# Performance work log

Measured on AMD Instinct MI355X. Metric: run time of the kernel, lower is better.

Reference implementation:

```python
import jax, jax.numpy as jnp
import numpy as np

HIDDEN_DIM = 256
N = 8192


def setup_inputs() -> dict:
    key = jax.random.key(0)
    k1, k2, k3, k4 = jax.random.split(key, 4)
    img = jax.random.normal(k1, (N, HIDDEN_DIM), dtype=jnp.float32)
    text = jax.random.normal(k2, (N, HIDDEN_DIM), dtype=jnp.float32)
    # nn.Linear(hidden_dim, hidden_dim, bias=False) weights, shape [out, in]
    scale = 1.0 / np.sqrt(HIDDEN_DIM)
    Wq = jax.random.uniform(k3, (HIDDEN_DIM, HIDDEN_DIM), dtype=jnp.float32, minval=-scale, maxval=scale)
    Wk = jax.random.uniform(k4, (HIDDEN_DIM, HIDDEN_DIM), dtype=jnp.float32, minval=-scale, maxval=scale)
    return {"img": img, "text": text, "Wq": Wq, "Wk": Wk}


def reference(img, text, Wq, Wk):
    d = img.shape[-1]
    norm_fact = 1.0 / jnp.sqrt(jnp.asarray(d, dtype=img.dtype))
    Q = img @ Wq.T                       # [N, D]
    K = text @ Wk.T                      # [N, D]
    scores = Q @ K.T                     # [N, N]
    # softmax over dim=1 (keys), then scaled by 1/sqrt(D)
    attn = jax.nn.softmax(scores, axis=1) * norm_fact
    out_img = attn @ img                 # [N, D]
    out_text = attn @ text               # [N, D]
    return (out_img, out_text)
```

## Files before the change

### kernel.cpp

```cpp
#include <hip/hip_runtime.h>

typedef unsigned short ushort_t;
typedef unsigned int uint_t;
typedef __attribute__((ext_vector_type(8))) short short8;
typedef __attribute__((ext_vector_type(8))) _Float16 half8;
typedef __attribute__((ext_vector_type(4))) _Float16 half4;
typedef __attribute__((ext_vector_type(4))) float float4v;

#define MFMA_BF16(a, b, c) __builtin_amdgcn_mfma_f32_16x16x32_bf16((a), (b), (c), 0, 0, 0)
#define MFMA_F16(a, b, c) __builtin_amdgcn_mfma_f32_16x16x32_f16((a), (b), (c), 0, 0, 0)

#define NQ 8192
#define DIM 256
#define DV 512

__device__ __forceinline__ ushort_t f2bf(float x) {
  union { float f; uint_t u; } v; v.f = x;
  return (ushort_t)((v.u + 0x7fffu + ((v.u >> 16) & 1u)) >> 16);
}
__device__ __forceinline__ float bf2f(ushort_t b) {
  union { uint_t u; float f; } v; v.u = ((uint_t)b) << 16;
  return v.f;
}

__device__ __forceinline__ half8 cvt8h(const float* p) {
  float4v a = *(const float4v*)p;
  float4v b = *(const float4v*)(p + 4);
  half8 r;
  r[0] = (_Float16)a[0]; r[1] = (_Float16)a[1];
  r[2] = (_Float16)a[2]; r[3] = (_Float16)a[3];
  r[4] = (_Float16)b[0]; r[5] = (_Float16)b[1];
  r[6] = (_Float16)b[2]; r[7] = (_Float16)b[3];
  return r;
}

__device__ __forceinline__ half8 as_h8(short8 s) {
  union { short8 s; half8 h; } u; u.s = s; return u.h;
}

__device__ __forceinline__ void load_lds_16(const void* g, void* l) {
  __builtin_amdgcn_global_load_lds(
      (const __attribute__((address_space(1))) uint_t*)g,
      (__attribute__((address_space(3))) uint_t*)l, 16, 0, 0);
}

__device__ __forceinline__ void barrier_vm0_lgkm0() {
  asm volatile("s_waitcnt vmcnt(0) lgkmcnt(0)\ns_barrier" ::: "memory");
}
__device__ __forceinline__ void barrier_lgkm0() {
  asm volatile("s_waitcnt lgkmcnt(0)\ns_barrier" ::: "memory");
}

__global__ __launch_bounds__(256) void wconv_kernel(
    const float* __restrict__ Wq, const float* __restrict__ Wk,
    _Float16* __restrict__ Whq, _Float16* __restrict__ Whk) {
  const int i = (blockIdx.x * 256 + threadIdx.x) * 8;
  half8 q = cvt8h(Wq + i);
  half8 k = cvt8h(Wk + i);
  *(half8*)(Whq + i) = q;
  *(half8*)(Whk + i) = k;
}

__global__ __launch_bounds__(256, 2) void pre_kernel(
    const float* __restrict__ img, const float* __restrict__ text,
    const _Float16* __restrict__ Whq, const _Float16* __restrict__ Whk,
    _Float16* __restrict__ Qh, _Float16* __restrict__ Kh,
    ushort_t* __restrict__ Vt) {
  __shared__ float tile[64][65];
  const int bid = blockIdx.x;
  const int tid = threadIdx.x;
  if (bid < 1024) {
    const int bx = bid & 127;
    const int by = (bid >> 7) & 3;
    const int bz = bid >> 9;
    const int lane = tid & 63;
    const int wv = tid >> 6;
    const int l16 = lane & 15;
    const int quad = lane >> 4;
    const float* A = bz ? text : img;
    const _Float16* W = bz ? Whk : Whq;
    _Float16* C = bz ? Kh : Qh;
    const int row = bx * 64 + wv * 16 + l16;
    const int colbase = by * 64;

    float4v acc[4];
#pragma unroll
    for (int c = 0; c < 4; ++c) acc[c] = (float4v){0.f, 0.f, 0.f, 0.f};
#pragma unroll
    for (int f = 0; f < 8; ++f) {
      const int k0 = f * 32 + quad * 8;
      half8 af = cvt8h(A + (size_t)row * DIM + k0);
#pragma unroll
      for (int c = 0; c < 4; ++c) {
        half8 bfr = *(const half8*)(W + (size_t)(colbase + c * 16 + l16) * DIM + k0);
        acc[c] = MFMA_F16(af, bfr, acc[c]);
      }
    }
    const int rbase = bx * 64 + wv * 16 + quad * 4;
#pragma unroll
    for (int c = 0; c < 4; ++c)
#pragma unroll
      for (int r = 0; r < 4; ++r)
        C[(size_t)(rbase + r) * DIM + colbase + c * 16 + l16] = (_Float16)acc[c][r];
  } else {
    const int vb = bid - 1024;
    const int n0 = (vb & 127) * 64;
    const int c0 = (vb >> 7) * 64;
    const float* src = (c0 < 256) ? img : text;
    const int cc0 = (c0 < 256) ? c0 : (c0 - 256);
#pragma unroll
    for (int i = 0; i < 4; ++i) {
      const int r = i * 16 + (tid >> 4);
      const int c = (tid & 15) * 4;
      *(float4v*)&tile[r][c] = *(const float4v*)(src + (size_t)(n0 + r) * DIM + cc0 + c);
    }
    __syncthreads();
    const int c = tid >> 2;
    const int seg = tid & 3;
    ushort_t tmp[16];
#pragma unroll
    for (int t = 0; t < 16; ++t) tmp[t] = f2bf(tile[seg * 16 + t][c]);
    ushort_t* dst = Vt + (size_t)(c0 + c) * NQ + n0 + seg * 16;
    *(short8*)dst = *(short8*)&tmp[0];
    *(short8*)(dst + 8) = *(short8*)&tmp[8];
  }
}

__device__ __forceinline__ void stage_K(const _Float16* __restrict__ Kh, int k0,
                                        ushort_t* dst, int tid, int wv) {
#pragma unroll
  for (int i = 0; i < 4; ++i) {
    const int chunk = i * 256 + tid;
    const int n = chunk >> 5;
    const int cs = (chunk & 31) ^ (n & 7);
    load_lds_16(Kh + (size_t)(k0 + n) * DIM + cs * 8,
                (char*)dst + (i * 256 + wv * 64) * 16);
  }
}
__device__ __forceinline__ void stage_V(const ushort_t* __restrict__ Vt, int k0,
                                        ushort_t* dst, int tid, int wv) {
#pragma unroll
  for (int i = 0; i < 8; ++i) {
    const int chunk = i * 256 + tid;
    const int vrow = chunk >> 2;
    const int dc = (chunk & 3) ^ ((vrow >> 1) & 3);
    load_lds_16(Vt + (size_t)vrow * NQ + k0 + dc * 8,
                (char*)dst + (i * 256 + wv * 64) * 16);
  }
}

__global__ __launch_bounds__(256, 2) void attn_kernel(
    const _Float16* __restrict__ Qh, const _Float16* __restrict__ Kh,
    const ushort_t* __restrict__ Vt, _Float16* __restrict__ pacc,
    float* __restrict__ pdenom, int kps, int ks) {
  extern __shared__ __align__(16) ushort_t smem[];
  ushort_t* ldsV = smem + 16384;

  const int tid = threadIdx.x;
  const int lane = tid & 63;
  const int wv = tid >> 6;
  const int l16 = lane & 15;
  const int quad = lane >> 4;
  const int id = blockIdx.x;
  const int split = id & (ks - 1);
  const int qtile = id / ks;
  const int kbeg = split * kps;
  const int sw2 = (l16 >> 1) & 3;
  const int swk = l16 & 7;

  short8 qf[8];
  {
    const _Float16* qptr = Qh + (size_t)(qtile * 64 + wv * 16 + l16) * DIM;
#pragma unroll
    for (int f = 0; f < 8; ++f)
      qf[f] = *(const short8*)(qptr + f * 32 + quad * 8);
  }

  float4v acc[4][8];
#pragma unroll
  for (int m = 0; m < 4; ++m)
#pragma unroll
    for (int c = 0; c < 8; ++c) acc[m][c] = (float4v){0.f, 0.f, 0.f, 0.f};
  float dacc[4] = {0.f, 0.f, 0.f, 0.f};

  const int ntiles = kps >> 5;

  stage_K(Kh, kbeg, smem, tid, wv);
  stage_V(Vt, kbeg, ldsV, tid, wv);

  for (int t = 0; t < ntiles; ++t) {
    const ushort_t* Kt = smem + (t & 1) * 8192;
    barrier_vm0_lgkm0();
    if (t + 1 < ntiles)
      stage_K(Kh, kbeg + (t + 1) * 32, smem + ((t + 1) & 1) * 8192, tid, wv);

    if (t > 0) {
      const ushort_t* Pprev = smem + 32768 + ((t - 1) & 1) * 2048;
      short8 pa[4];
#pragma unroll
      for (int m = 0; m < 4; ++m)
        pa[m] = *(const short8*)(Pprev + (m * 16 + l16) * 32 + (quad ^ sw2) * 8);
      __builtin_amdgcn_s_setprio(1);
#pragma unroll
      for (int c = 0; c < 8; ++c) {
        const int vcol = (wv * 8 + c) * 16 + l16;
        short8 vb = *(const short8*)(ldsV + vcol * 32 + (quad ^ sw2) * 8);
#pragma unroll
        for (int m = 0; m < 4; ++m)
          acc[m][c] = MFMA_BF16(pa[m], vb, acc[m][c]);
      }
      __builtin_amdgcn_s_setprio(0);
    }

    float4v s0 = (float4v){0.f, 0.f, 0.f, 0.f};
    float4v s1 = (float4v){0.f, 0.f, 0.f, 0.f};
    __builtin_amdgcn_s_setprio(1);
#pragma unroll
    for (int f = 0; f < 8; ++f) {
      const int cs = ((f * 4 + quad) ^ swk) * 8;
      short8 kb0 = *(const short8*)(Kt + l16 * DIM + cs);
      short8 kb1 = *(const short8*)(Kt + (l16 + 16) * DIM + cs);
      s0 = MFMA_F16(as_h8(qf[f]), as_h8(kb0), s0);
      s1 = MFMA_F16(as_h8(qf[f]), as_h8(kb1), s1);
    }
    __builtin_amdgcn_s_setprio(0);

    barrier_lgkm0();
    if (t >= 1) stage_V(Vt, kbeg + t * 32, ldsV, tid, wv);

    ushort_t* Pcur = smem + 32768 + (t & 1) * 2048;
    ushort_t pb0[4], pb1[4];
#pragma unroll
    for (int r = 0; r < 4; ++r) {
      pb0[r] = f2bf(__expf(s0[r]));
      pb1[r] = f2bf(__expf(s1[r]));
    }
#pragma unroll
    for (int r = 0; r < 4; ++r) {
      const int rb = wv * 16 + quad * 4 + r;
      const int swp = (rb >> 1) & 3;
      Pcur[rb * 32 + ((l16 >> 3) ^ swp) * 8 + (l16 & 7)] = pb0[r];
      Pcur[rb * 32 + ((2 + (l16 >> 3)) ^ swp) * 8 + (l16 & 7)] = pb1[r];
      dacc[r] += bf2f(pb0[r]) + bf2f(pb1[r]);
    }
  }

  barrier_vm0_lgkm0();
  {
    const ushort_t* Pprev = smem + 32768 + ((ntiles - 1) & 1) * 2048;
    short8 pa[4];
#pragma unroll
    for (int m = 0; m < 4; ++m)
      pa[m] = *(const short8*)(Pprev + (m * 16 + l16) * 32 + (quad ^ sw2) * 8);
#pragma unroll
    for (int c = 0; c < 8; ++c) {
      const int vcol = (wv * 8 + c) * 16 + l16;
      short8 vb = *(const short8*)(ldsV + vcol * 32 + (quad ^ sw2) * 8);
#pragma unroll
      for (int m = 0; m < 4; ++m)
        acc[m][c] = MFMA_BF16(pa[m], vb, acc[m][c]);
    }
  }

#pragma unroll
  for (int r = 0; r < 4; ++r) {
    float ts = dacc[r];
    ts += __shfl_xor(ts, 1);
    ts += __shfl_xor(ts, 2);
    ts += __shfl_xor(ts, 4);
    ts += __shfl_xor(ts, 8);
    dacc[r] = ts;
  }

  barrier_lgkm0();
  float* ldsD = (float*)smem;
  if (l16 == 0) {
#pragma unroll
    for (int r = 0; r < 4; ++r)
      ldsD[wv * 16 + quad * 4 + r] = dacc[r];
  }
  barrier_lgkm0();

  _Float16* pout = pacc + (size_t)split * ((size_t)NQ * DV);
#pragma unroll
  for (int m = 0; m < 4; ++m) {
    float invd[4];
#pragma unroll
    for (int r = 0; r < 4; ++r) invd[r] = 1.0f / ldsD[m * 16 + quad * 4 + r];
    const int rowbase = qtile * 64 + m * 16 + quad * 4;
#pragma unroll
    for (int c = 0; c < 8; ++c) {
      const int col = (wv * 8 + c) * 16 + l16;
#pragma unroll
      for (int r = 0; r < 4; ++r)
        pout[(size_t)(rowbase + r) * DV + col] = (_Float16)(acc[m][c][r] * invd[r]);
    }
  }
  if (l16 == 0) {
    const int rowbase = qtile * 64 + wv * 16 + quad * 4;
#pragma unroll
    for (int r = 0; r < 4; ++r)
      pdenom[split * NQ + rowbase + r] = dacc[r];
  }
}

__global__ __launch_bounds__(256) void combine_kernel(
    const _Float16* __restrict__ pacc, const float* __restrict__ pdenom,
    float* __restrict__ out, int ks) {
  const int idx = blockIdx.x * 256 + threadIdx.x;
  const int n = idx >> 6;
  const int c8 = (idx & 63) << 3;
  float s[8] = {0.f, 0.f, 0.f, 0.f, 0.f, 0.f, 0.f, 0.f};
  float dsum = 0.f;
  for (int sp = 0; sp < ks; ++sp) {
    const float d = pdenom[sp * NQ + n];
    half8 x = *(const half8*)(pacc + (size_t)sp * ((size_t)NQ * DV) + (size_t)n * DV + c8);
#pragma unroll
    for (int j = 0; j < 8; ++j) s[j] += d * (float)x[j];
    dsum += d;
  }
  const float scale = 1.0f / (16.0f * dsum);
  float4v lo = (float4v){s[0], s[1], s[2], s[3]} * scale;
  float4v hi = (float4v){s[4], s[5], s[6], s[7]} * scale;
  float* dst = (c8 < 256) ? (out + (size_t)n * DIM + c8)
                          : (out + (size_t)NQ * DIM + (size_t)n * DIM + (c8 - 256));
  *(float4v*)dst = lo;
  *(float4v*)(dst + 4) = hi;
}

extern "C" void kernel_launch(void* const* d_in, const int* in_sizes, int n_in,
                              void* d_out, int out_size, void* d_ws, size_t ws_size,
                              hipStream_t stream) {
  const float* img = (const float*)d_in[0];
  const float* text = (const float*)d_in[1];
  const float* Wq = (const float*)d_in[2];
  const float* Wk = (const float*)d_in[3];
  float* out = (float*)d_out;
  char* ws = (char*)d_ws;

  _Float16* Qh = (_Float16*)ws;
  _Float16* Kh = (_Float16*)(ws + ((size_t)4 << 20));
  ushort_t* Vt = (ushort_t*)(ws + ((size_t)8 << 20));
  const size_t accsz = (size_t)NQ * DV * sizeof(_Float16);
  const size_t base = (size_t)16 << 20;

  int ks = 4;
  if (ws_size < base + 4 * (accsz + NQ * sizeof(float))) ks = 2;
  _Float16* pacc = (_Float16*)(ws + base);
  float* pdenom = (float*)(ws + base + (size_t)ks * accsz);
  _Float16* Whq = (_Float16*)(ws + base);
  _Float16* Whk = Whq + DIM * DIM;

  hipLaunchKernelGGL(wconv_kernel, dim3(32), dim3(256), 0, stream,
                     Wq, Wk, Whq, Whk);
  hipLaunchKernelGGL(pre_kernel, dim3(2048), dim3(256), 0, stream,
                     img, text, Whq, Whk, Qh, Kh, Vt);
  hipLaunchKernelGGL(attn_kernel, dim3(128 * ks), dim3(256),
                     36864 * sizeof(ushort_t), stream,
                     Qh, Kh, Vt, pacc, pdenom, NQ / ks, ks);
  hipLaunchKernelGGL(combine_kernel, dim3((NQ * DV / 8) / 256), dim3(256), 0, stream,
                     pacc, pdenom, out, ks);
}
```

Baseline: 231.8 us.

## Specialize waves: two compute QK and partial PV, two do PV only

```diff
diff --git a/kernel.cpp b/kernel.cpp
--- a/kernel.cpp
+++ b/kernel.cpp
@@ -149,6 +149,48 @@
   }
 }
 
+template <int NCT>
+__device__ __forceinline__ void pv_step(float4v (&acc)[4][NCT],
+                                        const ushort_t* __restrict__ Pprev,
+                                        const ushort_t* __restrict__ ldsV,
+                                        int ctb, int l16, int quad, int sw2) {
+  short8 pa[4];
+#pragma unroll
+  for (int m = 0; m < 4; ++m)
+    pa[m] = *(const short8*)(Pprev + (m * 16 + l16) * 32 + (quad ^ sw2) * 8);
+  __builtin_amdgcn_s_setprio(1);
+#pragma unroll
+  for (int c = 0; c < NCT; ++c) {
+    const int vcol = (ctb + c) * 16 + l16;
+    short8 vb = *(const short8*)(ldsV + vcol * 32 + (quad ^ sw2) * 8);
+#pragma unroll
+    for (int m = 0; m < 4; ++m)
+      acc[m][c] = MFMA_BF16(pa[m], vb, acc[m][c]);
+  }
+  __builtin_amdgcn_s_setprio(0);
+}
+
+template <int NCT>
+__device__ __forceinline__ void write_out(const float4v (&acc)[4][NCT],
+                                          _Float16* __restrict__ pout,
+                                          const float* __restrict__ ldsD,
+                                          int ctb, int qtile, int l16, int quad) {
+#pragma unroll
+  for (int m = 0; m < 4; ++m) {
+    float invd[4];
+#pragma unroll
+    for (int r = 0; r < 4; ++r) invd[r] = 1.0f / ldsD[m * 16 + quad * 4 + r];
+    const int rowbase = qtile * 64 + m * 16 + quad * 4;
+#pragma unroll
+    for (int c = 0; c < NCT; ++c) {
+      const int col = (ctb + c) * 16 + l16;
+#pragma unroll
+      for (int r = 0; r < 4; ++r)
+        pout[(size_t)(rowbase + r) * DV + col] = (_Float16)(acc[m][c][r] * invd[r]);
+    }
+  }
+}
+
 __global__ __launch_bounds__(256, 2) void attn_kernel(
     const _Float16* __restrict__ Qh, const _Float16* __restrict__ Kh,
     const ushort_t* __restrict__ Vt, _Float16* __restrict__ pacc,
@@ -167,140 +209,141 @@
   const int kbeg = split * kps;
   const int sw2 = (l16 >> 1) & 3;
   const int swk = l16 & 7;
-
-  short8 qf[8];
-  {
-    const _Float16* qptr = Qh + (size_t)(qtile * 64 + wv * 16 + l16) * DIM;
-#pragma unroll
-    for (int f = 0; f < 8; ++f)
-      qf[f] = *(const short8*)(qptr + f * 32 + quad * 8);
-  }
-
-  float4v acc[4][8];
-#pragma unroll
-  for (int m = 0; m < 4; ++m)
-#pragma unroll
-    for (int c = 0; c < 8; ++c) acc[m][c] = (float4v){0.f, 0.f, 0.f, 0.f};
-  float dacc[4] = {0.f, 0.f, 0.f, 0.f};
-
   const int ntiles = kps >> 5;
+
+  _Float16* pout = pacc + (size_t)split * ((size_t)NQ * DV);
+  float* ldsD = (float*)smem;
 
   stage_K(Kh, kbeg, smem, tid, wv);
   stage_V(Vt, kbeg, ldsV, tid, wv);
 
-  for (int t = 0; t < ntiles; ++t) {
-    const ushort_t* Kt = smem + (t & 1) * 8192;
-    barrier_vm0_lgkm0();
-    if (t + 1 < ntiles)
-      stage_K(Kh, kbeg + (t + 1) * 32, smem + ((t + 1) & 1) * 8192, tid, wv);
-
-    if (t > 0) {
-      const ushort_t* Pprev = smem + 32768 + ((t - 1) & 1) * 2048;
-      short8 pa[4];
-#pragma unroll
-      for (int m = 0; m < 4; ++m)
-        pa[m] = *(const short8*)(Pprev + (m * 16 + l16) * 32 + (quad ^ sw2) * 8);
+  if (wv < 2) {
+    const int ctb = wv * 5;
+    short8 qf[2][8];
+#pragma unroll
+    for (int j = 0; j < 2; ++j) {
+      const _Float16* qptr =
+          Qh + (size_t)(qtile * 64 + (2 * wv + j) * 16 + l16) * DIM;
+#pragma unroll
+      for (int f = 0; f < 8; ++f)
+        qf[j][f] = *(const short8*)(qptr + f * 32 + quad * 8);
+    }
+    float4v acc[4][5];
+#pragma unroll
+    for (int m = 0; m < 4; ++m)
+#pragma unroll
+      for (int c = 0; c < 5; ++c) acc[m][c] = (float4v){0.f, 0.f, 0.f, 0.f};
+    float dacc[2][4];
+#pragma unroll
+    for (int j = 0; j < 2; ++j)
+#pragma unroll
+      for (int r = 0; r < 4; ++r) dacc[j][r] = 0.f;
+
+    for (int t = 0; t < ntiles; ++t) {
+      const ushort_t* Kt = smem + (t & 1) * 8192;
+      barrier_vm0_lgkm0();
+      if (t + 1 < ntiles)
+        stage_K(Kh, kbeg + (t + 1) * 32, smem + ((t + 1) & 1) * 8192, tid, wv);
+
+      if (t > 0)
+        pv_step<5>(acc, smem + 32768 + ((t - 1) & 1) * 2048, ldsV, ctb, l16,
+                   quad, sw2);
+
+      float4v s[2][2];
       __builtin_amdgcn_s_setprio(1);
 #pragma unroll
-      for (int c = 0; c < 8; ++c) {
-        const int vcol = (wv * 8 + c) * 16 + l16;
-        short8 vb = *(const short8*)(ldsV + vcol * 32 + (quad ^ sw2) * 8);
-#pragma unroll
-        for (int m = 0; m < 4; ++m)
-          acc[m][c] = MFMA_BF16(pa[m], vb, acc[m][c]);
+      for (int j = 0; j < 2; ++j) {
+        s[j][0] = (float4v){0.f, 0.f, 0.f, 0.f};
+        s[j][1] = (float4v){0.f, 0.f, 0.f, 0.f};
+#pragma unroll
+        for (int f = 0; f < 8; ++f) {
+          const int cs = ((f * 4 + quad) ^ swk) * 8;
+          short8 kb0 = *(const short8*)(Kt + l16 * DIM + cs);
+          short8 kb1 = *(const short8*)(Kt + (l16 + 16) * DIM + cs);
+          s[j][0] = MFMA_F16(as_h8(qf[j][f]), as_h8(kb0), s[j][0]);
+          s[j][1] = MFMA_F16(as_h8(qf[j][f]), as_h8(kb1), s[j][1]);
+        }
       }
       __builtin_amdgcn_s_setprio(0);
-    }
-
-    float4v s0 = (float4v){0.f, 0.f, 0.f, 0.f};
-    float4v s1 = (float4v){0.f, 0.f, 0.f, 0.f};
-    __builtin_amdgcn_s_setprio(1);
-#pragma unroll
-    for (int f = 0; f < 8; ++f) {
-      const int cs = ((f * 4 + quad) ^ swk) * 8;
-      short8 kb0 = *(const short8*)(Kt + l16 * DIM + cs);
-      short8 kb1 = *(const short8*)(Kt + (l16 + 16) * DIM + cs);
-      s0 = MFMA_F16(as_h8(qf[f]), as_h8(kb0), s0);
-      s1 = MFMA_F16(as_h8(qf[f]), as_h8(kb1), s1);
-    }
-    __builtin_amdgcn_s_setprio(0);
-
+
+      barrier_lgkm0();
+      if (t >= 1) stage_V(Vt, kbeg + t * 32, ldsV, tid, wv);
+
+      ushort_t* Pcur = smem + 32768 + (t & 1) * 2048;
+#pragma unroll
+      for (int j = 0; j < 2; ++j) {
+#pragma unroll
+        for (int r = 0; r < 4; ++r) {
+          const ushort_t pb0 = f2bf(__expf(s[j][0][r]));
+          const ushort_t pb1 = f2bf(__expf(s[j][1][r]));
+          const int rb = (2 * wv + j) * 16 + quad * 4 + r;
+          const int swp = (rb >> 1) & 3;
+          Pcur[rb * 32 + ((l16 >> 3) ^ swp) * 8 + (l16 & 7)] = pb0;
+          Pcur[rb * 32 + ((2 + (l16 >> 3)) ^ swp) * 8 + (l16 & 7)] = pb1;
+          dacc[j][r] += bf2f(pb0) + bf2f(pb1);
+        }
+      }
+    }
+
+    barrier_vm0_lgkm0();
+    pv_step<5>(acc, smem + 32768 + ((ntiles - 1) & 1) * 2048, ldsV, ctb, l16,
+               quad, sw2);
+#pragma unroll
+    for (int j = 0; j < 2; ++j)
+#pragma unroll
+      for (int r = 0; r < 4; ++r) {
+        float ts = dacc[j][r];
+        ts += __shfl_xor(ts, 1);
+        ts += __shfl_xor(ts, 2);
+        ts += __shfl_xor(ts, 4);
+        ts += __shfl_xor(ts, 8);
+        dacc[j][r] = ts;
+      }
     barrier_lgkm0();
-    if (t >= 1) stage_V(Vt, kbeg + t * 32, ldsV, tid, wv);
-
-    ushort_t* Pcur = smem + 32768 + (t & 1) * 2048;
-    ushort_t pb0[4], pb1[4];
-#pragma unroll
-    for (int r = 0; r < 4; ++r) {
-      pb0[r] = f2bf(__expf(s0[r]));
-      pb1[r] = f2bf(__expf(s1[r]));
-    }
-#pragma unroll
-    for (int r = 0; r < 4; ++r) {
-      const int rb = wv * 16 + quad * 4 + r;
-      const int swp = (rb >> 1) & 3;
-      Pcur[rb * 32 + ((l16 >> 3) ^ swp) * 8 + (l16 & 7)] = pb0[r];
-      Pcur[rb * 32 + ((2 + (l16 >> 3)) ^ swp) * 8 + (l16 & 7)] = pb1[r];
-      dacc[r] += bf2f(pb0[r]) + bf2f(pb1[r]);
-    }
-  }
-
-  barrier_vm0_lgkm0();
-  {
-    const ushort_t* Pprev = smem + 32768 + ((ntiles - 1) & 1) * 2048;
-    short8 pa[4];
+    if (l16 == 0) {
+#pragma unroll
+      for (int j = 0; j < 2; ++j)
+#pragma unroll
+        for (int r = 0; r < 4; ++r)
+          ldsD[(2 * wv + j) * 16 + quad * 4 + r] = dacc[j][r];
+    }
+    barrier_lgkm0();
+    write_out<5>(acc, pout, ldsD, ctb, qtile, l16, quad);
+    if (l16 == 0) {
+#pragma unroll
+      for (int j = 0; j < 2; ++j)
+#pragma unroll
+        for (int r = 0; r < 4; ++r)
+          pdenom[split * NQ + qtile * 64 + (2 * wv + j) * 16 + quad * 4 + r] =
+              dacc[j][r];
+    }
+  } else {
+    const int ctb = 10 + (wv - 2) * 11;
+    float4v acc[4][11];
 #pragma unroll
     for (int m = 0; m < 4; ++m)
-      pa[m] = *(const short8*)(Pprev + (m * 16 + l16) * 32 + (quad ^ sw2) * 8);
-#pragma unroll
-    for (int c = 0; c < 8; ++c) {
-      const int vcol = (wv * 8 + c) * 16 + l16;
-      short8 vb = *(const short8*)(ldsV + vcol * 32 + (quad ^ sw2) * 8);
-#pragma unroll
-      for (int m = 0; m < 4; ++m)
-        acc[m][c] = MFMA_BF16(pa[m], vb, acc[m][c]);
-    }
-  }
-
-#pragma unroll
-  for (int r = 0; r < 4; ++r) {
-    float ts = dacc[r];
-    ts += __shfl_xor(ts, 1);
-    ts += __shfl_xor(ts, 2);
-    ts += __shfl_xor(ts, 4);
-    ts += __shfl_xor(ts, 8);
-    dacc[r] = ts;
-  }
-
-  barrier_lgkm0();
-  float* ldsD = (float*)smem;
-  if (l16 == 0) {
-#pragma unroll
-    for (int r = 0; r < 4; ++r)
-      ldsD[wv * 16 + quad * 4 + r] = dacc[r];
-  }
-  barrier_lgkm0();
-
-  _Float16* pout = pacc + (size_t)split * ((size_t)NQ * DV);
-#pragma unroll
-  for (int m = 0; m < 4; ++m) {
-    float invd[4];
-#pragma unroll
-    for (int r = 0; r < 4; ++r) invd[r] = 1.0f / ldsD[m * 16 + quad * 4 + r];
-    const int rowbase = qtile * 64 + m * 16 + quad * 4;
-#pragma unroll
-    for (int c = 0; c < 8; ++c) {
-      const int col = (wv * 8 + c) * 16 + l16;
-#pragma unroll
-      for (int r = 0; r < 4; ++r)
-        pout[(size_t)(rowbase + r) * DV + col] = (_Float16)(acc[m][c][r] * invd[r]);
-    }
-  }
-  if (l16 == 0) {
-    const int rowbase = qtile * 64 + wv * 16 + quad * 4;
-#pragma unroll
-    for (int r = 0; r < 4; ++r)
-      pdenom[split * NQ + rowbase + r] = dacc[r];
+#pragma unroll
+      for (int c = 0; c < 11; ++c) acc[m][c] = (float4v){0.f, 0.f, 0.f, 0.f};
+
+    for (int t = 0; t < ntiles; ++t) {
+      barrier_vm0_lgkm0();
+      if (t + 1 < ntiles)
+        stage_K(Kh, kbeg + (t + 1) * 32, smem + ((t + 1) & 1) * 8192, tid, wv);
+
+      if (t > 0)
+        pv_step<11>(acc, smem + 32768 + ((t - 1) & 1) * 2048, ldsV, ctb, l16,
+                    quad, sw2);
+
+      barrier_lgkm0();
+      if (t >= 1) stage_V(Vt, kbeg + t * 32, ldsV, tid, wv);
+    }
+
+    barrier_vm0_lgkm0();
+    pv_step<11>(acc, smem + 32768 + ((ntiles - 1) & 1) * 2048, ldsV, ctb, l16,
+                quad, sw2);
+    barrier_lgkm0();
+    barrier_lgkm0();
+    write_out<11>(acc, pout, ldsD, ctb, qtile, l16, quad);
   }
 }
 
```

New measurement: 305.4 us. 1.32x slower.
